# Optimization experiments

Hardware: AMD Instinct MI355X
Metric: run time of the kernel (lower is better)

The kernel has to match this reference:

```python
import jax, jax.numpy as jnp
import numpy as np

B, T, E, D, A, EMB, V = 128, 96, 512, 512, 512, 512, 4096


def _linear_params(k, out_d, in_d):
    bound = 1.0 / np.sqrt(in_d)
    k1, k2 = jax.random.split(k)
    W = jax.random.uniform(k1, (out_d, in_d), minval=-bound, maxval=bound)
    b = jax.random.uniform(k2, (out_d,), minval=-bound, maxval=bound)
    return W, b


def setup_inputs() -> dict:
    key = jax.random.key(0)
    ks = jax.random.split(key, 16)
    W_enc, b_enc = _linear_params(ks[0], A, E)
    W_dec, b_dec = _linear_params(ks[1], A, D)
    W_full, b_full = _linear_params(ks[2], 1, A)
    W_init_h, b_init_h = _linear_params(ks[3], D, E)
    W_init_c, b_init_c = _linear_params(ks[4], D, E)
    W_fbeta, b_fbeta = _linear_params(ks[5], E, D)
    W_fc = jax.random.uniform(ks[6], (V, D), minval=-0.1, maxval=0.1)
    b_fc = jnp.zeros((V,), jnp.float32)
    emb_table = jax.random.uniform(ks[7], (V, EMB), minval=-0.1, maxval=0.1)
    W_ih, b_ih = _linear_params(ks[8], 4 * D, EMB + E)
    W_hh, b_hh = _linear_params(ks[9], 4 * D, D)
    encoder_out = jax.random.normal(ks[10], (B, E), jnp.float32)
    encoded_captions = jax.random.randint(ks[11], (B, T), 0, V)
    caption_lengths = jax.random.randint(ks[12], (B, 1), 1, T + 1)
    return dict(encoder_out=encoder_out, encoded_captions=encoded_captions,
                caption_lengths=caption_lengths,
                W_enc=W_enc, b_enc=b_enc, W_dec=W_dec, b_dec=b_dec,
                W_full=W_full, b_full=b_full,
                W_init_h=W_init_h, b_init_h=b_init_h,
                W_init_c=W_init_c, b_init_c=b_init_c,
                W_fbeta=W_fbeta, b_fbeta=b_fbeta,
                W_fc=W_fc, b_fc=b_fc, emb_table=emb_table,
                W_ih=W_ih, b_ih=b_ih, W_hh=W_hh, b_hh=b_hh)


def reference(encoder_out, encoded_captions, caption_lengths,
              W_enc, b_enc, W_dec, b_dec, W_full, b_full,
              W_init_h, b_init_h, W_init_c, b_init_c,
              W_fbeta, b_fbeta, W_fc, b_fc, emb_table,
              W_ih, b_ih, W_hh, b_hh):
    # sort by caption length, descending (as in torch forward)
    lens = caption_lengths[:, 0]
    order = jnp.argsort(-lens)
    enc = encoder_out[order]            # (B, E)
    caps = encoded_captions[order]      # (B, T)
    lens_s = lens[order]
    embeds = emb_table[caps]            # (B, T, EMB)
    h0 = enc @ W_init_h.T + b_init_h    # (B, D)
    c0 = enc @ W_init_c.T + b_init_c
    att1 = enc @ W_enc.T + b_enc        # (B, A), fixed over time
    # valid[t, i] == (i < batch_size_t), since lengths are sorted descending
    valid = (jnp.arange(T)[None, :] < lens_s[:, None]).T  # (T, B)

    def step(carry, xs):
        h, c = carry
        emb_t, v = xs                   # (B, EMB), (B,) bool
        att2 = h @ W_dec.T + b_dec      # (B, A)
        # additive attention over the batch dim (the actual math of My_attention on 2D input)
        scores = jax.nn.relu(att1[None, :, :] + att2[:, None, :]) @ W_full[0] + b_full[0]  # (B, B)
        scores = jnp.where(v[None, :], scores, -1e9)
        alpha = jax.nn.softmax(scores, axis=1)
        awe = alpha @ enc               # (B, E)
        gate = jax.nn.sigmoid(h @ W_fbeta.T + b_fbeta)
        awe = gate * awe
        x = jnp.concatenate([emb_t, awe], axis=1)  # (B, EMB+E)
        gates = x @ W_ih.T + b_ih + h @ W_hh.T + b_hh
        gi, gf, gg, go = jnp.split(gates, 4, axis=1)  # torch LSTMCell order: i,f,g,o
        gi, gf, go = jax.nn.sigmoid(gi), jax.nn.sigmoid(gf), jax.nn.sigmoid(go)
        gg = jnp.tanh(gg)
        c_new = gf * c + gi * gg
        h_new = go * jnp.tanh(c_new)
        preds = h_new @ W_fc.T + b_fc   # dropout is identity in eval
        vm = v[:, None]
        return (jnp.where(vm, h_new, h), jnp.where(vm, c_new, c)), jnp.where(vm, preds, 0.0)

    (_, _), preds = jax.lax.scan(jax.checkpoint(step), (h0, c0),
                                 (jnp.transpose(embeds, (1, 0, 2)), valid))
    # (B, T, V), rows in sorted order, zero-padded past each caption length
    # (torch pack_padded_sequence is a pure reordering/gather of exactly these entries)
    return jnp.transpose(preds, (1, 0, 2))
```

## Files before the change

kernel.cpp:

```cpp
#include <hip/hip_runtime.h>

#define Bsz  128
#define Tlen 96
#define Edim 512
#define Ddim 512
#define Adim 512
#define EMBd 512
#define Vdim 4096

__device__ __forceinline__ float sigm(float x) { return 1.0f / (1.0f + expf(-x)); }

__global__ void k_sort(const int* __restrict__ lens, int* __restrict__ order,
                       int* __restrict__ lens_s) {
    __shared__ int L[Bsz];
    int j = threadIdx.x;
    L[j] = lens[j];
    __syncthreads();
    int lj = L[j];
    int rank = 0;
    for (int m = 0; m < Bsz; ++m) {
        int lm = L[m];
        if (lm > lj || (lm == lj && m < j)) rank++;
    }
    order[rank] = j;
    lens_s[rank] = lj;
}

__global__ void k_gather(const float* __restrict__ enc_in,
                         const int* __restrict__ order, float* __restrict__ enc_s) {
    int i = blockIdx.x;
    int src = order[i];
    for (int d = threadIdx.x; d < Edim; d += 256)
        enc_s[i * Edim + d] = enc_in[src * Edim + d];
}

__device__ __forceinline__ void mm_tile(const float* __restrict__ act,
                                        const float* __restrict__ W,
                                        int K, int i0, float acc[4][4]) {
    __shared__ float sA[64][17];
    __shared__ float sB[64][17];
    int tid = threadIdx.x;
    int tx = tid & 15, ty = tid >> 4;
    for (int k0 = 0; k0 < K; k0 += 16) {
        {
            int idx = tid * 4;
            int row = idx >> 4;
            int kk = idx & 15;
            const float* p = act + (size_t)(i0 + row) * K + k0 + kk;
            float4 v = *reinterpret_cast<const float4*>(p);
            sA[row][kk + 0] = v.x; sA[row][kk + 1] = v.y;
            sA[row][kk + 2] = v.z; sA[row][kk + 3] = v.w;
        }
        {
            int idx = tid * 4;
            int row = idx >> 4;
            int kk = idx & 15;
            const float* p = W + (size_t)row * K + k0 + kk;
            float4 v = *reinterpret_cast<const float4*>(p);
            sB[row][kk + 0] = v.x; sB[row][kk + 1] = v.y;
            sB[row][kk + 2] = v.z; sB[row][kk + 3] = v.w;
        }
        __syncthreads();
#pragma unroll
        for (int kk = 0; kk < 16; ++kk) {
            float a[4], b[4];
#pragma unroll
            for (int r = 0; r < 4; ++r) a[r] = sA[ty * 4 + r][kk];
#pragma unroll
            for (int cidx = 0; cidx < 4; ++cidx) b[cidx] = sB[tx * 4 + cidx][kk];
#pragma unroll
            for (int r = 0; r < 4; ++r)
#pragma unroll
                for (int cidx = 0; cidx < 4; ++cidx)
                    acc[r][cidx] += a[r] * b[cidx];
        }
        __syncthreads();
    }
}

__global__ __launch_bounds__(256) void k_init(
    const float* __restrict__ enc_s,
    const float* __restrict__ W_init_h, const float* __restrict__ b_init_h,
    const float* __restrict__ W_init_c, const float* __restrict__ b_init_c,
    const float* __restrict__ W_enc, const float* __restrict__ b_enc,
    float* __restrict__ h, float* __restrict__ c, float* __restrict__ att1) {
    int j0 = blockIdx.x * 64;
    int i0 = blockIdx.y * 64;
    const float* W; const float* bias; float* out; int jl;
    if (j0 < 512)       { W = W_init_h; bias = b_init_h; out = h;    jl = j0; }
    else if (j0 < 1024) { W = W_init_c; bias = b_init_c; out = c;    jl = j0 - 512; }
    else                { W = W_enc;    bias = b_enc;    out = att1; jl = j0 - 1024; }
    float acc[4][4] = {};
    mm_tile(enc_s, W + (size_t)jl * Edim, Edim, i0, acc);
    int tx = threadIdx.x & 15, ty = threadIdx.x >> 4;
#pragma unroll
    for (int r = 0; r < 4; ++r)
#pragma unroll
        for (int cc = 0; cc < 4; ++cc) {
            int i = i0 + ty * 4 + r, j = jl + tx * 4 + cc;
            out[i * 512 + j] = acc[r][cc] + bias[j];
        }
}

__global__ __launch_bounds__(256) void k_stepA(
    const float* __restrict__ h,
    const float* __restrict__ W_fc, const float* __restrict__ b_fc,
    const float* __restrict__ W_dec, const float* __restrict__ b_dec,
    const float* __restrict__ W_fbeta, const float* __restrict__ b_fbeta,
    const float* __restrict__ W_hh, const float* __restrict__ b_hh,
    float* __restrict__ att2, float* __restrict__ gate, float* __restrict__ hh,
    float* __restrict__ out, const int* __restrict__ lens_s, int t) {
    int j0 = blockIdx.x * 64;
    int i0 = blockIdx.y * 64;
    int tx = threadIdx.x & 15, ty = threadIdx.x >> 4;
    if (j0 < 4096) {
        if (t == 0) return;
        float acc[4][4] = {};
        mm_tile(h, W_fc + (size_t)j0 * Ddim, Ddim, i0, acc);
        int tt = t - 1;
#pragma unroll
        for (int r = 0; r < 4; ++r) {
            int i = i0 + ty * 4 + r;
            bool valid = tt < lens_s[i];
#pragma unroll
            for (int cc = 0; cc < 4; ++cc) {
                int j = j0 + tx * 4 + cc;
                float v = valid ? (acc[r][cc] + b_fc[j]) : 0.0f;
                out[((size_t)i * Tlen + tt) * Vdim + j] = v;
            }
        }
    } else if (j0 < 4608) {
        float acc[4][4] = {};
        int jl = j0 - 4096;
        mm_tile(h, W_dec + (size_t)jl * Ddim, Ddim, i0, acc);
#pragma unroll
        for (int r = 0; r < 4; ++r)
#pragma unroll
            for (int cc = 0; cc < 4; ++cc) {
                int i = i0 + ty * 4 + r, j = jl + tx * 4 + cc;
                att2[i * 512 + j] = acc[r][cc] + b_dec[j];
            }
    } else if (j0 < 5120) {
        float acc[4][4] = {};
        int jl = j0 - 4608;
        mm_tile(h, W_fbeta + (size_t)jl * Ddim, Ddim, i0, acc);
#pragma unroll
        for (int r = 0; r < 4; ++r)
#pragma unroll
            for (int cc = 0; cc < 4; ++cc) {
                int i = i0 + ty * 4 + r, j = jl + tx * 4 + cc;
                gate[i * 512 + j] = sigm(acc[r][cc] + b_fbeta[j]);
            }
    } else {
        float acc[4][4] = {};
        int jl = j0 - 5120;
        mm_tile(h, W_hh + (size_t)jl * Ddim, Ddim, i0, acc);
#pragma unroll
        for (int r = 0; r < 4; ++r)
#pragma unroll
            for (int cc = 0; cc < 4; ++cc) {
                int i = i0 + ty * 4 + r, j = jl + tx * 4 + cc;
                hh[i * 2048 + j] = acc[r][cc] + b_hh[j];
            }
    }
}

__global__ __launch_bounds__(256) void k_stepB(
    const float* __restrict__ att1, const float* __restrict__ att2,
    const float* __restrict__ enc_s,
    const float* __restrict__ W_full, const float* __restrict__ b_full,
    const float* __restrict__ gate, const float* __restrict__ emb_table,
    const int* __restrict__ caps, const int* __restrict__ order,
    const int* __restrict__ lens_s, float* __restrict__ x, int t) {
    int i = blockIdx.x;
    int tid = threadIdx.x;
    __shared__ float sA2[512];
    __shared__ float sWF[512];
    __shared__ float sSC[128];
    __shared__ float sRed[2];
    for (int d = tid; d < 512; d += 256) {
        sA2[d] = att2[i * 512 + d];
        sWF[d] = W_full[d];
    }
    __syncthreads();
    if (tid < 128) {
        int j = tid;
        const float* a1 = att1 + j * 512;
        float acc = 0.0f;
        for (int k = 0; k < 512; ++k) {
            float v = a1[k] + sA2[k];
            acc += fmaxf(v, 0.0f) * sWF[k];
        }
        float sc = acc + b_full[0];
        if (t >= lens_s[j]) sc = -1000000000.0f;
        sSC[j] = sc;
    }
    __syncthreads();
    if (tid < 64) {
        float m = fmaxf(sSC[tid], sSC[tid + 64]);
        for (int o = 32; o; o >>= 1) m = fmaxf(m, __shfl_down(m, o));
        if (tid == 0) sRed[0] = m;
    }
    __syncthreads();
    if (tid < 128) sSC[tid] = expf(sSC[tid] - sRed[0]);
    __syncthreads();
    if (tid < 64) {
        float s = sSC[tid] + sSC[tid + 64];
        for (int o = 32; o; o >>= 1) s += __shfl_down(s, o);
        if (tid == 0) sRed[1] = s;
    }
    __syncthreads();
    float inv = 1.0f / sRed[1];
    int cap = caps[order[i] * Tlen + t];
    for (int d = tid; d < 512; d += 256) {
        float acc = 0.0f;
        for (int j = 0; j < 128; ++j) acc += sSC[j] * enc_s[j * 512 + d];
        acc *= inv;
        x[i * 1024 + 512 + d] = gate[i * 512 + d] * acc;
        x[i * 1024 + d] = emb_table[(size_t)cap * EMBd + d];
    }
}

__global__ __launch_bounds__(256) void k_stepC(
    const float* __restrict__ x, const float* __restrict__ W_ih,
    const float* __restrict__ b_ih, const float* __restrict__ hh,
    float* __restrict__ gates) {
    int j0 = blockIdx.x * 64;
    int i0 = blockIdx.y * 64;
    float acc[4][4] = {};
    mm_tile(x, W_ih + (size_t)j0 * 1024, 1024, i0, acc);
    int tx = threadIdx.x & 15, ty = threadIdx.x >> 4;
#pragma unroll
    for (int r = 0; r < 4; ++r)
#pragma unroll
        for (int cc = 0; cc < 4; ++cc) {
            int i = i0 + ty * 4 + r, j = j0 + tx * 4 + cc;
            gates[i * 2048 + j] = acc[r][cc] + b_ih[j] + hh[i * 2048 + j];
        }
}

__global__ void k_lstm(const float* __restrict__ gates, float* __restrict__ h,
                       float* __restrict__ c, const int* __restrict__ lens_s, int t) {
    int idx = blockIdx.x * 256 + threadIdx.x;
    int i = idx >> 9, d = idx & 511;
    if (t >= lens_s[i]) return;
    float gi = sigm(gates[i * 2048 + d]);
    float gf = sigm(gates[i * 2048 + 512 + d]);
    float gg = tanhf(gates[i * 2048 + 1024 + d]);
    float go = sigm(gates[i * 2048 + 1536 + d]);
    float cn = gf * c[idx] + gi * gg;
    float hn = go * tanhf(cn);
    c[idx] = cn;
    h[idx] = hn;
}

extern "C" void kernel_launch(void* const* d_in, const int* in_sizes, int n_in,
                              void* d_out, int out_size, void* d_ws, size_t ws_size,
                              hipStream_t stream) {
    const float* encoder_out = (const float*)d_in[0];
    const int* caps = (const int*)d_in[1];
    const int* lens = (const int*)d_in[2];
    const float* W_enc = (const float*)d_in[3];
    const float* b_enc = (const float*)d_in[4];
    const float* W_dec = (const float*)d_in[5];
    const float* b_dec = (const float*)d_in[6];
    const float* W_full = (const float*)d_in[7];
    const float* b_full = (const float*)d_in[8];
    const float* W_init_h = (const float*)d_in[9];
    const float* b_init_h = (const float*)d_in[10];
    const float* W_init_c = (const float*)d_in[11];
    const float* b_init_c = (const float*)d_in[12];
    const float* W_fbeta = (const float*)d_in[13];
    const float* b_fbeta = (const float*)d_in[14];
    const float* W_fc = (const float*)d_in[15];
    const float* b_fc = (const float*)d_in[16];
    const float* emb_table = (const float*)d_in[17];
    const float* W_ih = (const float*)d_in[18];
    const float* b_ih = (const float*)d_in[19];
    const float* W_hh = (const float*)d_in[20];
    const float* b_hh = (const float*)d_in[21];
    float* out = (float*)d_out;

    char* p = (char*)d_ws;
    auto alloc = [&](size_t bytes) {
        void* r = (void*)p;
        p += (bytes + 255) & ~(size_t)255;
        return r;
    };
    int* order = (int*)alloc(Bsz * 4);
    int* lens_s = (int*)alloc(Bsz * 4);
    float* enc_s = (float*)alloc(Bsz * Edim * 4);
    float* att1 = (float*)alloc(Bsz * Adim * 4);
    float* h = (float*)alloc(Bsz * Ddim * 4);
    float* c = (float*)alloc(Bsz * Ddim * 4);
    float* att2 = (float*)alloc(Bsz * Adim * 4);
    float* gate = (float*)alloc(Bsz * Ddim * 4);
    float* hh = (float*)alloc(Bsz * 2048 * 4);
    float* x = (float*)alloc(Bsz * 1024 * 4);
    float* gates = (float*)alloc(Bsz * 2048 * 4);

    k_sort<<<1, 128, 0, stream>>>(lens, order, lens_s);
    k_gather<<<Bsz, 256, 0, stream>>>(encoder_out, order, enc_s);
    k_init<<<dim3(24, 2), 256, 0, stream>>>(enc_s, W_init_h, b_init_h, W_init_c,
                                            b_init_c, W_enc, b_enc, h, c, att1);
    for (int t = 0; t < Tlen; ++t) {
        k_stepA<<<dim3(112, 2), 256, 0, stream>>>(h, W_fc, b_fc, W_dec, b_dec,
                                                  W_fbeta, b_fbeta, W_hh, b_hh,
                                                  att2, gate, hh, out, lens_s, t);
        k_stepB<<<Bsz, 256, 0, stream>>>(att1, att2, enc_s, W_full, b_full, gate,
                                         emb_table, caps, order, lens_s, x, t);
        k_stepC<<<dim3(32, 2), 256, 0, stream>>>(x, W_ih, b_ih, hh, gates);
        k_lstm<<<256, 256, 0, stream>>>(gates, h, c, lens_s, t);
    }
    k_stepA<<<dim3(64, 2), 256, 0, stream>>>(h, W_fc, b_fc, W_dec, b_dec, W_fbeta,
                                             b_fbeta, W_hh, b_hh, att2, gate, hh,
                                             out, lens_s, Tlen);
}
```

Baseline: 13.43 ms.

## Hoist vocab projection out of recurrence into one batched bf16 MFMA GEMM

```diff
diff --git a/kernel.cpp b/kernel.cpp
--- a/kernel.cpp
+++ b/kernel.cpp
@@ -8,7 +8,15 @@
 #define EMBd 512
 #define Vdim 4096
 
+typedef __attribute__((ext_vector_type(8))) short short8v;
+typedef __attribute__((ext_vector_type(4))) float f32x4;
+
 __device__ __forceinline__ float sigm(float x) { return 1.0f / (1.0f + expf(-x)); }
+__device__ __forceinline__ unsigned short f2bf(float f) {
+    unsigned int x = __float_as_uint(f);
+    unsigned int r = (x + 0x7FFFu + ((x >> 16) & 1u)) >> 16;
+    return (unsigned short)r;
+}
 
 __global__ void k_sort(const int* __restrict__ lens, int* __restrict__ order,
                        int* __restrict__ lens_s) {
@@ -32,6 +40,12 @@
     int src = order[i];
     for (int d = threadIdx.x; d < Edim; d += 256)
         enc_s[i * Edim + d] = enc_in[src * Edim + d];
+}
+
+__global__ void k_cvtW(const float* __restrict__ W, unsigned short* __restrict__ O,
+                       int n) {
+    int i = blockIdx.x * 256 + threadIdx.x;
+    if (i < n) O[i] = f2bf(W[i]);
 }
 
 __device__ __forceinline__ void mm_tile(const float* __restrict__ act,
@@ -104,45 +118,26 @@
 
 __global__ __launch_bounds__(256) void k_stepA(
     const float* __restrict__ h,
-    const float* __restrict__ W_fc, const float* __restrict__ b_fc,
     const float* __restrict__ W_dec, const float* __restrict__ b_dec,
     const float* __restrict__ W_fbeta, const float* __restrict__ b_fbeta,
     const float* __restrict__ W_hh, const float* __restrict__ b_hh,
-    float* __restrict__ att2, float* __restrict__ gate, float* __restrict__ hh,
-    float* __restrict__ out, const int* __restrict__ lens_s, int t) {
+    float* __restrict__ att2, float* __restrict__ gate, float* __restrict__ hh) {
     int j0 = blockIdx.x * 64;
     int i0 = blockIdx.y * 64;
     int tx = threadIdx.x & 15, ty = threadIdx.x >> 4;
-    if (j0 < 4096) {
-        if (t == 0) return;
+    if (j0 < 512) {
         float acc[4][4] = {};
-        mm_tile(h, W_fc + (size_t)j0 * Ddim, Ddim, i0, acc);
-        int tt = t - 1;
-#pragma unroll
-        for (int r = 0; r < 4; ++r) {
-            int i = i0 + ty * 4 + r;
-            bool valid = tt < lens_s[i];
+        mm_tile(h, W_dec + (size_t)j0 * Ddim, Ddim, i0, acc);
+#pragma unroll
+        for (int r = 0; r < 4; ++r)
 #pragma unroll
             for (int cc = 0; cc < 4; ++cc) {
-                int j = j0 + tx * 4 + cc;
-                float v = valid ? (acc[r][cc] + b_fc[j]) : 0.0f;
-                out[((size_t)i * Tlen + tt) * Vdim + j] = v;
-            }
-        }
-    } else if (j0 < 4608) {
-        float acc[4][4] = {};
-        int jl = j0 - 4096;
-        mm_tile(h, W_dec + (size_t)jl * Ddim, Ddim, i0, acc);
-#pragma unroll
-        for (int r = 0; r < 4; ++r)
-#pragma unroll
-            for (int cc = 0; cc < 4; ++cc) {
-                int i = i0 + ty * 4 + r, j = jl + tx * 4 + cc;
+                int i = i0 + ty * 4 + r, j = j0 + tx * 4 + cc;
                 att2[i * 512 + j] = acc[r][cc] + b_dec[j];
             }
-    } else if (j0 < 5120) {
+    } else if (j0 < 1024) {
         float acc[4][4] = {};
-        int jl = j0 - 4608;
+        int jl = j0 - 512;
         mm_tile(h, W_fbeta + (size_t)jl * Ddim, Ddim, i0, acc);
 #pragma unroll
         for (int r = 0; r < 4; ++r)
@@ -153,7 +148,7 @@
             }
     } else {
         float acc[4][4] = {};
-        int jl = j0 - 5120;
+        int jl = j0 - 1024;
         mm_tile(h, W_hh + (size_t)jl * Ddim, Ddim, i0, acc);
 #pragma unroll
         for (int r = 0; r < 4; ++r)
@@ -240,18 +235,73 @@
 }
 
 __global__ void k_lstm(const float* __restrict__ gates, float* __restrict__ h,
-                       float* __restrict__ c, const int* __restrict__ lens_s, int t) {
+                       float* __restrict__ c, const int* __restrict__ lens_s,
+                       unsigned short* __restrict__ h_hist, int t) {
     int idx = blockIdx.x * 256 + threadIdx.x;
     int i = idx >> 9, d = idx & 511;
-    if (t >= lens_s[i]) return;
-    float gi = sigm(gates[i * 2048 + d]);
-    float gf = sigm(gates[i * 2048 + 512 + d]);
-    float gg = tanhf(gates[i * 2048 + 1024 + d]);
-    float go = sigm(gates[i * 2048 + 1536 + d]);
-    float cn = gf * c[idx] + gi * gg;
-    float hn = go * tanhf(cn);
-    c[idx] = cn;
-    h[idx] = hn;
+    float hv;
+    if (t < lens_s[i]) {
+        float gi = sigm(gates[i * 2048 + d]);
+        float gf = sigm(gates[i * 2048 + 512 + d]);
+        float gg = tanhf(gates[i * 2048 + 1024 + d]);
+        float go = sigm(gates[i * 2048 + 1536 + d]);
+        float cn = gf * c[idx] + gi * gg;
+        hv = go * tanhf(cn);
+        c[idx] = cn;
+        h[idx] = hv;
+    } else {
+        hv = h[idx];
+    }
+    h_hist[(size_t)t * (Bsz * 512) + idx] = f2bf(hv);
+}
+
+__global__ __launch_bounds__(256) void k_preds(
+    const unsigned short* __restrict__ hh16, const unsigned short* __restrict__ wfc16,
+    const float* __restrict__ b_fc, const int* __restrict__ lens_s,
+    float* __restrict__ out) {
+    int nb = blockIdx.x;
+    int mb = blockIdx.y;
+    int wid = threadIdx.x >> 6;
+    int lane = threadIdx.x & 63;
+    int wr = wid >> 1, wc = wid & 1;
+    int m_wave = mb * 128 + wr * 64;
+    int n_wave = nb * 128 + wc * 64;
+    int r = lane & 15, g = lane >> 4;
+    f32x4 acc[4][4];
+#pragma unroll
+    for (int a = 0; a < 4; ++a)
+#pragma unroll
+        for (int b = 0; b < 4; ++b) acc[a][b] = (f32x4){0.f, 0.f, 0.f, 0.f};
+    for (int kk = 0; kk < 512; kk += 32) {
+        short8v av[4], bv[4];
+#pragma unroll
+        for (int mf = 0; mf < 4; ++mf)
+            av[mf] = *reinterpret_cast<const short8v*>(
+                &hh16[(size_t)(m_wave + mf * 16 + r) * 512 + kk + g * 8]);
+#pragma unroll
+        for (int nf = 0; nf < 4; ++nf)
+            bv[nf] = *reinterpret_cast<const short8v*>(
+                &wfc16[(size_t)(n_wave + nf * 16 + r) * 512 + kk + g * 8]);
+#pragma unroll
+        for (int mf = 0; mf < 4; ++mf)
+#pragma unroll
+            for (int nf = 0; nf < 4; ++nf)
+                acc[mf][nf] = __builtin_amdgcn_mfma_f32_16x16x32_bf16(
+                    av[mf], bv[nf], acc[mf][nf], 0, 0, 0);
+    }
+#pragma unroll
+    for (int mf = 0; mf < 4; ++mf)
+#pragma unroll
+        for (int nf = 0; nf < 4; ++nf)
+#pragma unroll
+            for (int reg = 0; reg < 4; ++reg) {
+                int m = m_wave + mf * 16 + g * 4 + reg;
+                int col = n_wave + nf * 16 + r;
+                int t = m >> 7, i = m & 127;
+                bool valid = t < lens_s[i];
+                out[((size_t)i * Tlen + t) * Vdim + col] =
+                    valid ? acc[mf][nf][reg] + b_fc[col] : 0.0f;
+            }
 }
 
 extern "C" void kernel_launch(void* const* d_in, const int* in_sizes, int n_in,
@@ -298,21 +348,21 @@
     float* hh = (float*)alloc(Bsz * 2048 * 4);
     float* x = (float*)alloc(Bsz * 1024 * 4);
     float* gates = (float*)alloc(Bsz * 2048 * 4);
+    unsigned short* h_hist = (unsigned short*)alloc((size_t)Tlen * Bsz * 512 * 2);
+    unsigned short* wfc16 = (unsigned short*)alloc((size_t)Vdim * Ddim * 2);
 
     k_sort<<<1, 128, 0, stream>>>(lens, order, lens_s);
     k_gather<<<Bsz, 256, 0, stream>>>(encoder_out, order, enc_s);
+    k_cvtW<<<(Vdim * Ddim + 255) / 256, 256, 0, stream>>>(W_fc, wfc16, Vdim * Ddim);
     k_init<<<dim3(24, 2), 256, 0, stream>>>(enc_s, W_init_h, b_init_h, W_init_c,
                                             b_init_c, W_enc, b_enc, h, c, att1);
     for (int t = 0; t < Tlen; ++t) {
-        k_stepA<<<dim3(112, 2), 256, 0, stream>>>(h, W_fc, b_fc, W_dec, b_dec,
-                                                  W_fbeta, b_fbeta, W_hh, b_hh,
-                                                  att2, gate, hh, out, lens_s, t);
+        k_stepA<<<dim3(48, 2), 256, 0, stream>>>(h, W_dec, b_dec, W_fbeta, b_fbeta,
+                                                 W_hh, b_hh, att2, gate, hh);
         k_stepB<<<Bsz, 256, 0, stream>>>(att1, att2, enc_s, W_full, b_full, gate,
                                          emb_table, caps, order, lens_s, x, t);
         k_stepC<<<dim3(32, 2), 256, 0, stream>>>(x, W_ih, b_ih, hh, gates);
-        k_lstm<<<256, 256, 0, stream>>>(gates, h, c, lens_s, t);
-    }
-    k_stepA<<<dim3(64, 2), 256, 0, stream>>>(h, W_fc, b_fc, W_dec, b_dec, W_fbeta,
-                                             b_fbeta, W_hh, b_hh, att2, gate, hh,
-                                             out, lens_s, Tlen);
-}
+        k_lstm<<<256, 256, 0, stream>>>(gates, h, c, lens_s, h_hist, t);
+    }
+    k_preds<<<dim3(32, 96), 256, 0, stream>>>(h_hist, wfc16, b_fc, lens_s, out);
+}
```

Result: no change. 13.23 ms (-1.4%).
